# Optimization experiments

Measured on AMD Instinct MI355X. Metric: run time of the kernel, lower is better.

## Reference

```python
import jax, jax.numpy as jnp
import numpy as np

# ---- static configuration (mirrors RPN init + FPN anchor generator) ----
IMG_H = 800; IMG_W = 800
STRIDES = [4, 8, 16, 32, 64]
FEAT_SIZES = [(200, 200), (100, 100), (50, 50), (25, 25), (13, 13)]
SCALES = [32.0, 64.0, 128.0, 256.0, 512.0]
RATIOS = [0.5, 1.0, 2.0]
NUM_ANCHORS_PER_LEVEL = [len(RATIOS) * h * w for h, w in FEAT_SIZES]
A_TOTAL = sum(NUM_ANCHORS_PER_LEVEL)  # 159882
BATCH = 4
PRE_NMS_TOP_N = 1000   # _pre_nms_top_n['testing']
POST_NMS_TOP_N = 1000  # _post_nms_top_n['testing']
NMS_THRESH = 0.7
SCORE_THRESH = 0.0
MIN_SIZE = 0.001
BBOX_XFORM_CLIP = float(np.log(1000.0 / 16.0))  # torchvision BoxCoder clamp


def make_anchors():
    out = []
    for (fh, fw), stride, scale in zip(FEAT_SIZES, STRIDES, SCALES):
        base = np.array([[-scale * np.sqrt(1.0 / ar) / 2, -scale * np.sqrt(ar) / 2,
                          scale * np.sqrt(1.0 / ar) / 2, scale * np.sqrt(ar) / 2]
                         for ar in RATIOS], np.float32)  # [A,4]
        sx = (np.arange(fw, dtype=np.float32) + 0.5) * stride
        sy = (np.arange(fh, dtype=np.float32) + 0.5) * stride
        yy, xx = np.meshgrid(sy, sx, indexing='ij')
        shifts = np.stack([xx, yy, xx, yy], axis=-1).reshape(-1, 1, 4)  # [HW,1,4]
        out.append((shifts + base[None]).reshape(-1, 4))  # (H,W,A) ordering
    return np.concatenate(out, axis=0).astype(np.float32)


def setup_inputs() -> dict:
    key = jax.random.key(0)
    k1, k2 = jax.random.split(key)
    objectness = jax.random.normal(k1, (BATCH, A_TOTAL), jnp.float32)
    pred_bbox_deltas = 0.2 * jax.random.normal(k2, (BATCH, A_TOTAL, 4), jnp.float32)
    anchors = jnp.asarray(make_anchors())
    return {"objectness": objectness, "pred_bbox_deltas": pred_bbox_deltas, "anchors": anchors}


def decode_boxes(deltas, anchors):
    # BoxCoder.decode with weights (1,1,1,1)
    wa = anchors[:, 2] - anchors[:, 0]
    ha = anchors[:, 3] - anchors[:, 1]
    cxa = anchors[:, 0] + 0.5 * wa
    cya = anchors[:, 1] + 0.5 * ha
    dx, dy = deltas[..., 0], deltas[..., 1]
    dw = jnp.minimum(deltas[..., 2], BBOX_XFORM_CLIP)
    dh = jnp.minimum(deltas[..., 3], BBOX_XFORM_CLIP)
    cx = dx * wa + cxa
    cy = dy * ha + cya
    w = jnp.exp(dw) * wa
    h = jnp.exp(dh) * ha
    return jnp.stack([cx - 0.5 * w, cy - 0.5 * h, cx + 0.5 * w, cy + 0.5 * h], axis=-1)


def top_n_idx(obj):
    # _get_top_n_idx: per-level top-k with running offset
    idxs = []
    off = 0
    for n in NUM_ANCHORS_PER_LEVEL:
        k = min(PRE_NMS_TOP_N, n)
        _, ti = jax.lax.top_k(obj[:, off:off + n], k)
        idxs.append(ti + off)
        off += n
    return jnp.concatenate(idxs, axis=1)


def pairwise_iou(b):
    area = (b[:, 2] - b[:, 0]) * (b[:, 3] - b[:, 1])
    lt = jnp.maximum(b[:, None, :2], b[None, :, :2])
    rb = jnp.minimum(b[:, None, 2:], b[None, :, 2:])
    wh = jnp.clip(rb - lt, 0.0)
    inter = wh[..., 0] * wh[..., 1]
    return inter / (area[:, None] + area[None, :] - inter)


def nms_single(boxes, scores, levels):
    # clip_boxes_to_image
    x1 = jnp.clip(boxes[:, 0], 0.0, IMG_W)
    y1 = jnp.clip(boxes[:, 1], 0.0, IMG_H)
    x2 = jnp.clip(boxes[:, 2], 0.0, IMG_W)
    y2 = jnp.clip(boxes[:, 3], 0.0, IMG_H)
    boxes = jnp.stack([x1, y1, x2, y2], axis=-1)
    # remove_small_boxes + score_thresh, expressed as a static mask
    valid = (x2 - x1 >= MIN_SIZE) & (y2 - y1 >= MIN_SIZE) & (scores >= SCORE_THRESH)
    # batched_nms trick: offset boxes per level so cross-level IoU is 0
    max_coord = jnp.max(boxes)
    off = levels.astype(boxes.dtype) * (max_coord + 1.0)
    nb = boxes + off[:, None]
    s = jnp.where(valid, scores, -jnp.inf)
    order = jnp.argsort(-s)
    b = nb[order]
    K = b.shape[0]
    iou = pairwise_iou(b)  # [K,K]
    keep0 = valid[order]
    ar = jnp.arange(K)
    def body(i, keep):
        sup = (iou[i] > NMS_THRESH) & (ar > i)
        return jnp.where(keep[i], keep & ~sup, keep)
    keep = jax.lax.fori_loop(0, K, body, keep0)  # greedy NMS
    kept_scores = jnp.where(keep, s[order], -jnp.inf)
    sel = jnp.argsort(-kept_scores)[:POST_NMS_TOP_N]  # stable: preserves score order
    fvalid = jnp.take(keep, sel)
    fb = jnp.take(boxes[order], sel, axis=0)
    fs = jnp.take(scores[order], sel)
    fb = jnp.where(fvalid[:, None], fb, 0.0)  # pad slots zeroed
    fs = jnp.where(fvalid, fs, 0.0)
    return fb, fs


def reference(objectness, pred_bbox_deltas, anchors):
    proposals = decode_boxes(pred_bbox_deltas, anchors)  # [N, A, 4]
    idx = top_n_idx(objectness)  # [N, K]
    levels = jnp.concatenate([jnp.full((n,), i, jnp.int32)
                              for i, n in enumerate(NUM_ANCHORS_PER_LEVEL)])
    bi = jnp.arange(objectness.shape[0])[:, None]
    sc = jax.nn.sigmoid(objectness[bi, idx])
    lv = levels[idx]
    pr = proposals[bi, idx]
    boxes, scores = jax.vmap(nms_single)(pr, sc, lv)
    return boxes, scores  # [N, POST_NMS_TOP_N, 4], [N, POST_NMS_TOP_N]
```

## Files before the change

### kernel.cpp

```cpp
#include <hip/hip_runtime.h>
#include <math.h>

#define BATCH 4
#define A_TOTAL 159882
#define K_TOT 4507
#define N_WORDS 71
#define POST_N 1000

#define OFF_SEL      0u
#define OFF_SKEY     72192u
#define OFF_BOXES    216576u
#define OFF_SCORE    505088u
#define OFF_MAXC     577280u
#define OFF_BOXESS   577536u
#define OFF_NBS      866048u
#define OFF_SCORES   1154560u
#define OFF_SUPINIT  1226752u
#define OFF_MASK     1229056u

__device__ const int d_LVL_N[5]   = {120000, 30000, 7500, 1875, 507};
__device__ const int d_LVL_OFF[5] = {0, 120000, 150000, 157500, 159375};
__device__ const int d_LVL_K[5]   = {1000, 1000, 1000, 1000, 507};
__device__ const int d_CAT_OFF[5] = {0, 1000, 2000, 3000, 4000};

__device__ __forceinline__ float fadd_(float a, float b) { return __fadd_rn(a, b); }
__device__ __forceinline__ float fsub_(float a, float b) { return __fadd_rn(a, -b); }
__device__ __forceinline__ float fmul_(float a, float b) { return __fmul_rn(a, b); }

__device__ __forceinline__ unsigned flipf(float f) {
  unsigned u = __float_as_uint(f);
  return (u & 0x80000000u) ? ~u : (u | 0x80000000u);
}

__device__ __forceinline__ unsigned long long readlane64(unsigned long long v, int l) {
  unsigned lo = (unsigned)__builtin_amdgcn_readlane((int)(unsigned)(v & 0xffffffffull), l);
  unsigned hi = (unsigned)__builtin_amdgcn_readlane((int)(unsigned)(v >> 32), l);
  return ((unsigned long long)hi << 32) | (unsigned long long)lo;
}

__device__ __forceinline__ unsigned long long shflxor64(unsigned long long v, int msk) {
  unsigned lo = __shfl_xor((unsigned)(v & 0xffffffffull), msk, 64);
  unsigned hi = __shfl_xor((unsigned)(v >> 32), msk, 64);
  return ((unsigned long long)hi << 32) | (unsigned long long)lo;
}

__device__ void suffix_and_find(unsigned* hist, unsigned kcur,
                                unsigned* s_bucket, unsigned* s_knew, int tid) {
  for (int off = 1; off < 2048; off <<= 1) {
    unsigned v0 = hist[tid] + ((tid + off) < 2048 ? hist[tid + off] : 0u);
    unsigned v1 = hist[tid + 1024] + ((tid + 1024 + off) < 2048 ? hist[tid + 1024 + off] : 0u);
    __syncthreads();
    hist[tid] = v0; hist[tid + 1024] = v1;
    __syncthreads();
  }
  for (int q = 0; q < 2; ++q) {
    int idx = tid + q * 1024;
    unsigned s0 = hist[idx];
    unsigned s1 = (idx + 1 < 2048) ? hist[idx + 1] : 0u;
    if (s0 >= kcur && s1 < kcur) { *s_bucket = (unsigned)idx; *s_knew = kcur - s1; }
  }
  __syncthreads();
}

__global__ __launch_bounds__(1024) void topk_kernel(const float* __restrict__ obj,
                                                    int* __restrict__ selAnchor) {
  __shared__ unsigned hist[2048];
  __shared__ unsigned long long buf[2048];
  __shared__ unsigned s_bucket, s_knew, s_cnt;
  const int tid = threadIdx.x;
  const int bid = blockIdx.x;
  const int b = bid / 5, l = bid % 5;
  const int n = d_LVL_N[l];
  const int aoff = d_LVL_OFF[l];
  const unsigned kk = (unsigned)d_LVL_K[l];
  const float* src = obj + (size_t)b * A_TOTAL + aoff;

  hist[tid] = 0; hist[tid + 1024] = 0;
  __syncthreads();
  for (int i = tid; i < n; i += 1024) atomicAdd(&hist[flipf(src[i]) >> 21], 1u);
  __syncthreads();
  suffix_and_find(hist, kk, &s_bucket, &s_knew, tid);
  unsigned B1 = s_bucket, k2 = s_knew;
  __syncthreads();

  hist[tid] = 0; hist[tid + 1024] = 0;
  __syncthreads();
  for (int i = tid; i < n; i += 1024) {
    unsigned u = flipf(src[i]);
    if ((u >> 21) == B1) atomicAdd(&hist[(u >> 10) & 2047u], 1u);
  }
  __syncthreads();
  suffix_and_find(hist, k2, &s_bucket, &s_knew, tid);
  unsigned B2 = s_bucket, k3 = s_knew;
  __syncthreads();

  hist[tid] = 0; hist[tid + 1024] = 0;
  __syncthreads();
  unsigned pfx = (B1 << 11) | B2;
  for (int i = tid; i < n; i += 1024) {
    unsigned u = flipf(src[i]);
    if ((u >> 10) == pfx) atomicAdd(&hist[u & 1023u], 1u);
  }
  __syncthreads();
  suffix_and_find(hist, k3, &s_bucket, &s_knew, tid);
  unsigned T = (pfx << 10) | s_bucket;

  if (tid == 0) s_cnt = 0;
  __syncthreads();
  for (int i = tid; i < n; i += 1024) {
    unsigned u = flipf(src[i]);
    if (u >= T) {
      unsigned p = atomicAdd(&s_cnt, 1u);
      if (p < 2048u) buf[p] = ((unsigned long long)u << 32) | (unsigned long long)(~(unsigned)i);
    }
  }
  __syncthreads();
  unsigned cnt = s_cnt; if (cnt > 2048u) cnt = 2048u;
  for (int i = tid; i < 2048; i += 1024) if ((unsigned)i >= cnt) buf[i] = 0ull;
  for (unsigned kq = 2; kq <= 2048; kq <<= 1) {
    for (unsigned j = kq >> 1; j; j >>= 1) {
      __syncthreads();
      unsigned t = (unsigned)tid;
      unsigned i0 = ((t & ~(j - 1)) << 1) | (t & (j - 1));
      unsigned i1 = i0 | j;
      unsigned long long a = buf[i0], c = buf[i1];
      bool up = ((i0 & kq) == 0);
      if (up ? (a < c) : (a > c)) { buf[i0] = c; buf[i1] = a; }
    }
  }
  __syncthreads();
  if ((unsigned)tid < kk) {
    unsigned long long key = buf[tid];
    unsigned lidx = ~(unsigned)(key & 0xffffffffull);
    selAnchor[b * K_TOT + d_CAT_OFF[l] + tid] = aoff + (int)lidx;
  }
}

__global__ __launch_bounds__(512) void decode_kernel(
    const float* __restrict__ obj, const float* __restrict__ deltas,
    const float* __restrict__ anchors, const int* __restrict__ selAnchor,
    unsigned long long* __restrict__ skey, float4* __restrict__ boxes,
    float* __restrict__ score, float* __restrict__ maxc) {
  __shared__ float red[512];
  const int b = blockIdx.x;
  const int tid = threadIdx.x;
  float mymax = 0.0f;
  for (int pos = tid; pos < K_TOT; pos += 512) {
    int a = selAnchor[b * K_TOT + pos];
    float4 an = ((const float4*)anchors)[a];
    float4 dl = ((const float4*)deltas)[(size_t)b * A_TOTAL + a];
    float o = obj[(size_t)b * A_TOTAL + a];
    float wa = fsub_(an.z, an.x), ha = fsub_(an.w, an.y);
    float cxa = fadd_(an.x, fmul_(0.5f, wa));
    float cya = fadd_(an.y, fmul_(0.5f, ha));
    const float CLIP = (float)4.135166556742356;
    float dw = fminf(dl.z, CLIP), dh = fminf(dl.w, CLIP);
    float cx = fadd_(fmul_(dl.x, wa), cxa);
    float cy = fadd_(fmul_(dl.y, ha), cya);
    float w = fmul_((float)exp((double)dw), wa);
    float h = fmul_((float)exp((double)dh), ha);
    float x1 = fsub_(cx, fmul_(0.5f, w));
    float y1 = fsub_(cy, fmul_(0.5f, h));
    float x2 = fadd_(cx, fmul_(0.5f, w));
    float y2 = fadd_(cy, fmul_(0.5f, h));
    x1 = fminf(fmaxf(x1, 0.f), 800.f);
    y1 = fminf(fmaxf(y1, 0.f), 800.f);
    x2 = fminf(fmaxf(x2, 0.f), 800.f);
    y2 = fminf(fmaxf(y2, 0.f), 800.f);
    bool valid = (fsub_(x2, x1) >= 0.001f) && (fsub_(y2, y1) >= 0.001f);
    float s = (float)(1.0 / (1.0 + exp(-(double)o)));
    boxes[b * K_TOT + pos] = make_float4(x1, y1, x2, y2);
    score[b * K_TOT + pos] = s;
    float sm = valid ? s : -INFINITY;
    skey[b * K_TOT + pos] =
        ((unsigned long long)flipf(sm) << 32) | (unsigned long long)(~(unsigned)pos);
    mymax = fmaxf(mymax, fmaxf(fmaxf(x1, y1), fmaxf(x2, y2)));
  }
  red[tid] = mymax;
  __syncthreads();
  for (int s2 = 256; s2 > 0; s2 >>= 1) {
    if (tid < s2) red[tid] = fmaxf(red[tid], red[tid + s2]);
    __syncthreads();
  }
  if (tid == 0) maxc[b] = red[0];
}

__global__ __launch_bounds__(1024) void sort_kernel(
    const unsigned long long* __restrict__ skey, const float4* __restrict__ boxes,
    const float* __restrict__ score, const float* __restrict__ maxc,
    float4* __restrict__ boxesS, float4* __restrict__ nbS,
    float* __restrict__ scoreS, unsigned long long* __restrict__ supInit) {
  __shared__ unsigned long long keys[8192];
  const int b = blockIdx.x;
  const int tid = threadIdx.x;
  for (int t = tid; t < 8192; t += 1024)
    keys[t] = (t < K_TOT) ? skey[b * K_TOT + t] : 0ull;
  for (unsigned kq = 2; kq <= 8192; kq <<= 1) {
    for (unsigned j = kq >> 1; j; j >>= 1) {
      __syncthreads();
      for (unsigned t = (unsigned)tid; t < 4096; t += 1024) {
        unsigned i0 = ((t & ~(j - 1)) << 1) | (t & (j - 1));
        unsigned i1 = i0 | j;
        unsigned long long a = keys[i0], c = keys[i1];
        bool up = ((i0 & kq) == 0);
        if (up ? (a < c) : (a > c)) { keys[i0] = c; keys[i1] = a; }
      }
    }
  }
  __syncthreads();
  float mc1 = fadd_(maxc[b], 1.0f);
  for (int t = tid; t < 8192; t += 1024) {
    unsigned long long key = keys[t];
    bool inr = t < K_TOT;
    unsigned pos = ~(unsigned)(key & 0xffffffffull);
    bool valid = inr && ((unsigned)(key >> 32) != 0x007FFFFFu);
    if (inr) {
      float4 bx = boxes[b * K_TOT + pos];
      boxesS[b * K_TOT + t] = bx;
      int lvl = (int)(pos / 1000u);
      float offv = fmul_((float)lvl, mc1);
      nbS[b * K_TOT + t] = make_float4(fadd_(bx.x, offv), fadd_(bx.y, offv),
                                       fadd_(bx.z, offv), fadd_(bx.w, offv));
      scoreS[b * K_TOT + t] = score[b * K_TOT + pos];
    }
    unsigned long long bal = __ballot(valid);
    if (t < N_WORDS * 64 && (threadIdx.x & 63) == 0)
      supInit[b * N_WORDS + (t >> 6)] = ~bal;
  }
}

__global__ __launch_bounds__(64) void mask_kernel(const float4* __restrict__ nbS,
                                                  unsigned long long* __restrict__ mask) {
  const int b = blockIdx.y;
  int rem = blockIdx.x;
  int ib = 0;
  while (rem >= N_WORDS - ib) { rem -= (N_WORDS - ib); ++ib; }
  const int jb = ib + rem;
  __shared__ float4 jbox[64];
  __shared__ float jarea[64];
  const int lane = threadIdx.x;
  const int j0 = jb * 64;
  {
    int jj = j0 + lane;
    float4 bj = (jj < K_TOT) ? nbS[(size_t)b * K_TOT + jj]
                             : make_float4(-1e30f, -1e30f, -1e30f, -1e30f);
    jbox[lane] = bj;
    jarea[lane] = fmul_(fsub_(bj.z, bj.x), fsub_(bj.w, bj.y));
  }
  __syncthreads();
  const int i = ib * 64 + lane;
  if (i >= K_TOT) return;
  float4 bi = nbS[(size_t)b * K_TOT + i];
  float ai = fmul_(fsub_(bi.z, bi.x), fsub_(bi.w, bi.y));
  unsigned long long bits = 0ull;
  int jmax = K_TOT - j0; if (jmax > 64) jmax = 64;
  for (int q = 0; q < jmax; ++q) {
    int j = j0 + q;
    if (j <= i) continue;
    float4 bj = jbox[q];
    float ltx = fmaxf(bi.x, bj.x), lty = fmaxf(bi.y, bj.y);
    float rbx = fminf(bi.z, bj.z), rby = fminf(bi.w, bj.w);
    float wx = fmaxf(fsub_(rbx, ltx), 0.f), wy = fmaxf(fsub_(rby, lty), 0.f);
    float inter = fmul_(wx, wy);
    float uni = fsub_(fadd_(ai, jarea[q]), inter);
    float iou = inter / uni;
    if (iou > 0.7f) bits |= (1ull << q);
  }
  mask[((size_t)b * K_TOT + i) * N_WORDS + jb] = bits;
}

__global__ __launch_bounds__(64, 1) void scan_kernel(
    const unsigned long long* __restrict__ mask,
    const unsigned long long* __restrict__ supInit,
    const float4* __restrict__ boxesS, const float* __restrict__ scoreS,
    float* __restrict__ out) {
  __shared__ unsigned short keptIdx[POST_N];
  const int b = blockIdx.x;
  const int lane = threadIdx.x;
  const unsigned long long* m = mask + (size_t)b * K_TOT * N_WORDS;
  unsigned long long supA = supInit[b * N_WORDS + lane];
  unsigned long long supB = (lane < N_WORDS - 64) ? supInit[b * N_WORDS + 64 + lane] : ~0ull;
  float4* ob = (float4*)(out + (size_t)b * POST_N * 4);
  float* os = out + 4 * POST_N * 4 + (size_t)b * POST_N;
  const int lane2 = (lane + 64 < N_WORDS) ? (lane + 64) : lane;
  int c = 0;
  unsigned long long rw_cur = (lane < K_TOT) ? m[(size_t)lane * N_WORDS] : 0ull;
  for (int w = 0; w < N_WORDS; ++w) {
    unsigned long long rw_next = 0ull;
    if (w + 1 < N_WORDS) {
      int i1 = (w + 1) * 64 + lane;
      if (i1 < K_TOT) rw_next = m[(size_t)i1 * N_WORDS + (w + 1)];
    }
    if (w == 64) {
      for (int j = 0; j < N_WORDS - 64; ++j) {
        unsigned long long acc = 0ull;
        for (int base = 0; base < c; base += 64) {
          int k2 = base + lane;
          unsigned long long v2 = 0ull;
          if (k2 < c) v2 = m[(size_t)keptIdx[k2] * N_WORDS + 64 + j];
          acc |= v2;
        }
        for (int msk = 32; msk > 0; msk >>= 1) acc |= shflxor64(acc, msk);
        if (lane == j) supB |= acc;
      }
    }
    unsigned long long v = (w < 64) ? supA : supB;
    int srcl = (w < 64) ? w : (w - 64);
    unsigned long long scur = readlane64(v, srcl);
    unsigned long long avail0 = ~scur;
    unsigned long long keptm = 0ull;

    if (w < 64) {
      int tq[64];
      unsigned long long dA[64];
      unsigned long long av = avail0;
      if (avail0) {
#pragma unroll
        for (int q = 0; q < 64; ++q) {
          unsigned long long avq = av ? av : 1ull;
          tq[q] = __builtin_ctzll(avq);
          av &= av - 1ull;
          const unsigned long long* rp = m + (size_t)(w * 64 + tq[q]) * N_WORDS;
          asm volatile("global_load_dwordx2 %0, %1, off" : "=&v"(dA[q]) : "v"(rp + lane));
        }
      }
      __builtin_amdgcn_sched_barrier(0);
      unsigned long long avail = avail0;
      while (avail) {
        int t = __builtin_ctzll(avail);
        keptm |= (1ull << t);
        unsigned long long rw = readlane64(rw_cur, t);
        avail &= ~(rw | (1ull << t));
      }
      int nk = __popcll(keptm);
      if (keptm) {
        int pos = c + (int)__popcll(keptm & ((1ull << lane) - 1ull));
        if (((keptm >> lane) & 1ull) && pos < POST_N)
          keptIdx[pos] = (unsigned short)(w * 64 + lane);
      }
      c += nk;
      if (c >= POST_N) break;
      if (avail0) {
        asm volatile("s_waitcnt vmcnt(0)" ::: "memory");
        __builtin_amdgcn_sched_barrier(0);
        unsigned long long acc0 = 0ull;
#pragma unroll
        for (int q = 0; q < 64; ++q) {
          unsigned long long sel = ((keptm >> tq[q]) & 1ull) ? ~0ull : 0ull;
          acc0 |= dA[q] & sel;
        }
        supA |= acc0;
      }
    } else {
      unsigned long long avail = avail0;
      while (avail) {
        int t = __builtin_ctzll(avail);
        keptm |= (1ull << t);
        unsigned long long rw = readlane64(rw_cur, t);
        avail &= ~(rw | (1ull << t));
      }
      int nk = __popcll(keptm);
      if (keptm) {
        int pos = c + (int)__popcll(keptm & ((1ull << lane) - 1ull));
        if (((keptm >> lane) & 1ull) && pos < POST_N)
          keptIdx[pos] = (unsigned short)(w * 64 + lane);
      }
      c += nk;
      if (c >= POST_N) break;
      if (w + 1 >= N_WORDS) break;
      unsigned long long km = keptm;
      while (km != 0ull) {
        int ts[16];
        unsigned long long vm[16];
#pragma unroll
        for (int q = 0; q < 16; ++q) {
          unsigned long long kms = km ? km : 1ull;
          ts[q] = __builtin_ctzll(kms);
          vm[q] = km ? ~0ull : 0ull;
          km &= km - 1ull;
        }
        unsigned long long dA2[16], dB2[16];
#pragma unroll
        for (int q = 0; q < 16; ++q) {
          const unsigned long long* row = m + (size_t)(w * 64 + ts[q]) * N_WORDS;
          dA2[q] = row[lane];
          dB2[q] = row[lane2];
        }
        __builtin_amdgcn_sched_barrier(0);
        unsigned long long acc0 = 0ull, acc1 = 0ull;
#pragma unroll
        for (int q = 0; q < 16; ++q) {
          acc0 |= dA2[q] & vm[q];
          acc1 |= dB2[q] & vm[q];
        }
        supA |= acc0; supB |= acc1;
      }
    }
    rw_cur = rw_next;
  }
  __syncthreads();
  for (int t2 = lane; t2 < c && t2 < POST_N; t2 += 64) {
    int i = keptIdx[t2];
    ob[t2] = boxesS[(size_t)b * K_TOT + i];
    os[t2] = scoreS[(size_t)b * K_TOT + i];
  }
  for (int t2 = (c < POST_N ? c : POST_N) + lane; t2 < POST_N; t2 += 64) {
    ob[t2] = make_float4(0.f, 0.f, 0.f, 0.f);
    os[t2] = 0.f;
  }
}

extern "C" void kernel_launch(void* const* d_in, const int* in_sizes, int n_in,
                              void* d_out, int out_size, void* d_ws, size_t ws_size,
                              hipStream_t stream) {
  const float* obj = (const float*)d_in[0];
  const float* deltas = (const float*)d_in[1];
  const float* anchors = (const float*)d_in[2];
  float* out = (float*)d_out;
  char* ws = (char*)d_ws;

  int* selAnchor = (int*)(ws + OFF_SEL);
  unsigned long long* skey = (unsigned long long*)(ws + OFF_SKEY);
  float4* boxes = (float4*)(ws + OFF_BOXES);
  float* score = (float*)(ws + OFF_SCORE);
  float* maxc = (float*)(ws + OFF_MAXC);
  float4* boxesS = (float4*)(ws + OFF_BOXESS);
  float4* nbS = (float4*)(ws + OFF_NBS);
  float* scoreS = (float*)(ws + OFF_SCORES);
  unsigned long long* supInit = (unsigned long long*)(ws + OFF_SUPINIT);
  unsigned long long* mask = (unsigned long long*)(ws + OFF_MASK);

  hipLaunchKernelGGL(topk_kernel, dim3(BATCH * 5), dim3(1024), 0, stream, obj, selAnchor);
  hipLaunchKernelGGL(decode_kernel, dim3(BATCH), dim3(512), 0, stream,
                     obj, deltas, anchors, selAnchor, skey, boxes, score, maxc);
  hipLaunchKernelGGL(sort_kernel, dim3(BATCH), dim3(1024), 0, stream,
                     skey, boxes, score, maxc, boxesS, nbS, scoreS, supInit);
  hipLaunchKernelGGL(mask_kernel, dim3(N_WORDS * (N_WORDS + 1) / 2, BATCH), dim3(64), 0, stream,
                     nbS, mask);
  hipLaunchKernelGGL(scan_kernel, dim3(BATCH), dim3(64), 0, stream,
                     mask, supInit, boxesS, scoreS, out);
}
```

Baseline: 423.8 us.

## Rework top-k selection: replicated histograms, wave scan, rank-sort instead of bitonic

The per-level top-k kernel now spreads the first histogram pass over four padded copies to cut atomic contention. The block-wide suffix scan is replaced by a single-wave scan with shuffles. Candidates are split into strict-greater and tie sets, ties resolved by index with a wave min-reduction. The final order comes from an O(k^2) rank count instead of a 2048-element bitonic sort. This removes many block barriers but adds quadratic shared reads per thread and a serial tie-resolution loop when ties occur.

```diff
diff --git a/kernel.cpp b/kernel.cpp
--- a/kernel.cpp
+++ b/kernel.cpp
@@ -44,29 +44,44 @@
   return ((unsigned long long)hi << 32) | (unsigned long long)lo;
 }
 
-__device__ void suffix_and_find(unsigned* hist, unsigned kcur,
-                                unsigned* s_bucket, unsigned* s_knew, int tid) {
-  for (int off = 1; off < 2048; off <<= 1) {
-    unsigned v0 = hist[tid] + ((tid + off) < 2048 ? hist[tid + off] : 0u);
-    unsigned v1 = hist[tid + 1024] + ((tid + 1024 + off) < 2048 ? hist[tid + 1024 + off] : 0u);
-    __syncthreads();
-    hist[tid] = v0; hist[tid + 1024] = v1;
-    __syncthreads();
-  }
-  for (int q = 0; q < 2; ++q) {
-    int idx = tid + q * 1024;
-    unsigned s0 = hist[idx];
-    unsigned s1 = (idx + 1 < 2048) ? hist[idx + 1] : 0u;
-    if (s0 >= kcur && s1 < kcur) { *s_bucket = (unsigned)idx; *s_knew = kcur - s1; }
+#define HCOPIES 4
+#define HSTRIDE 2049
+#define TIE_CAP 2048
+
+__device__ __forceinline__ void suffix_find_wave(const unsigned* hist, unsigned kcur,
+                                                 unsigned* s_bucket, unsigned* s_knew,
+                                                 int tid) {
+  if (tid < 64) {
+    const int lane = tid;
+    unsigned ch[32];
+    unsigned csum = 0;
+#pragma unroll
+    for (int j = 0; j < 32; ++j) { ch[j] = hist[lane * 32 + j]; csum += ch[j]; }
+    unsigned cs = csum;
+    for (int off = 1; off < 64; off <<= 1) {
+      unsigned nb = __shfl_down(cs, off, 64);
+      cs += (lane + off < 64) ? nb : 0u;
+    }
+    unsigned running = cs - csum;
+#pragma unroll
+    for (int j = 31; j >= 0; --j) {
+      unsigned newrun = running + ch[j];
+      if (newrun >= kcur && running < kcur) {
+        *s_bucket = (unsigned)(lane * 32 + j);
+        *s_knew = kcur - running;
+      }
+      running = newrun;
+    }
   }
   __syncthreads();
 }
 
 __global__ __launch_bounds__(1024) void topk_kernel(const float* __restrict__ obj,
                                                     int* __restrict__ selAnchor) {
-  __shared__ unsigned hist[2048];
-  __shared__ unsigned long long buf[2048];
-  __shared__ unsigned s_bucket, s_knew, s_cnt;
+  __shared__ unsigned hist[HCOPIES * HSTRIDE];
+  __shared__ unsigned tieA[TIE_CAP];
+  __shared__ unsigned long long selK[1024];
+  __shared__ unsigned s_bucket, s_knew, s_ngt, s_ntie;
   const int tid = threadIdx.x;
   const int bid = blockIdx.x;
   const int b = bid / 5, l = bid % 5;
@@ -74,27 +89,33 @@
   const int aoff = d_LVL_OFF[l];
   const unsigned kk = (unsigned)d_LVL_K[l];
   const float* src = obj + (size_t)b * A_TOTAL + aoff;
-
-  hist[tid] = 0; hist[tid + 1024] = 0;
-  __syncthreads();
-  for (int i = tid; i < n; i += 1024) atomicAdd(&hist[flipf(src[i]) >> 21], 1u);
-  __syncthreads();
-  suffix_and_find(hist, kk, &s_bucket, &s_knew, tid);
+  int* outp = selAnchor + b * K_TOT + d_CAT_OFF[l];
+  const int wcopy = (tid >> 6) & (HCOPIES - 1);
+
+  for (int i = tid; i < HCOPIES * HSTRIDE; i += 1024) hist[i] = 0;
+  __syncthreads();
+  for (int i = tid; i < n; i += 1024)
+    atomicAdd(&hist[wcopy * HSTRIDE + (flipf(src[i]) >> 21)], 1u);
+  __syncthreads();
+  for (int i = tid; i < 2048; i += 1024)
+    hist[i] = hist[i] + hist[HSTRIDE + i] + hist[2 * HSTRIDE + i] + hist[3 * HSTRIDE + i];
+  __syncthreads();
+  suffix_find_wave(hist, kk, &s_bucket, &s_knew, tid);
   unsigned B1 = s_bucket, k2 = s_knew;
   __syncthreads();
 
-  hist[tid] = 0; hist[tid + 1024] = 0;
+  for (int i = tid; i < 2048; i += 1024) hist[i] = 0;
   __syncthreads();
   for (int i = tid; i < n; i += 1024) {
     unsigned u = flipf(src[i]);
     if ((u >> 21) == B1) atomicAdd(&hist[(u >> 10) & 2047u], 1u);
   }
   __syncthreads();
-  suffix_and_find(hist, k2, &s_bucket, &s_knew, tid);
+  suffix_find_wave(hist, k2, &s_bucket, &s_knew, tid);
   unsigned B2 = s_bucket, k3 = s_knew;
   __syncthreads();
 
-  hist[tid] = 0; hist[tid + 1024] = 0;
+  for (int i = tid; i < 2048; i += 1024) hist[i] = 0;
   __syncthreads();
   unsigned pfx = (B1 << 11) | B2;
   for (int i = tid; i < n; i += 1024) {
@@ -102,37 +123,57 @@
     if ((u >> 10) == pfx) atomicAdd(&hist[u & 1023u], 1u);
   }
   __syncthreads();
-  suffix_and_find(hist, k3, &s_bucket, &s_knew, tid);
+  suffix_find_wave(hist, k3, &s_bucket, &s_knew, tid);
   unsigned T = (pfx << 10) | s_bucket;
 
-  if (tid == 0) s_cnt = 0;
+  if (tid == 0) { s_ngt = 0; s_ntie = 0; }
   __syncthreads();
   for (int i = tid; i < n; i += 1024) {
     unsigned u = flipf(src[i]);
-    if (u >= T) {
-      unsigned p = atomicAdd(&s_cnt, 1u);
-      if (p < 2048u) buf[p] = ((unsigned long long)u << 32) | (unsigned long long)(~(unsigned)i);
-    }
-  }
-  __syncthreads();
-  unsigned cnt = s_cnt; if (cnt > 2048u) cnt = 2048u;
-  for (int i = tid; i < 2048; i += 1024) if ((unsigned)i >= cnt) buf[i] = 0ull;
-  for (unsigned kq = 2; kq <= 2048; kq <<= 1) {
-    for (unsigned j = kq >> 1; j; j >>= 1) {
-      __syncthreads();
-      unsigned t = (unsigned)tid;
-      unsigned i0 = ((t & ~(j - 1)) << 1) | (t & (j - 1));
-      unsigned i1 = i0 | j;
-      unsigned long long a = buf[i0], c = buf[i1];
-      bool up = ((i0 & kq) == 0);
-      if (up ? (a < c) : (a > c)) { buf[i0] = c; buf[i1] = a; }
-    }
-  }
-  __syncthreads();
-  if ((unsigned)tid < kk) {
-    unsigned long long key = buf[tid];
-    unsigned lidx = ~(unsigned)(key & 0xffffffffull);
-    selAnchor[b * K_TOT + d_CAT_OFF[l] + tid] = aoff + (int)lidx;
+    if (u > T) {
+      unsigned p = atomicAdd(&s_ngt, 1u);
+      selK[p] = ((unsigned long long)u << 32) | (unsigned)(~(unsigned)i);
+    } else if (u == T) {
+      unsigned q = atomicAdd(&s_ntie, 1u);
+      if (q < TIE_CAP) tieA[q] = (unsigned)i;
+    }
+  }
+  __syncthreads();
+  const unsigned ngt = s_ngt, ntie = s_ntie;
+  const unsigned need = kk - ngt;
+  if (ntie == need) {
+    for (unsigned q = tid; q < ntie; q += 1024)
+      selK[ngt + q] = ((unsigned long long)T << 32) | (unsigned)(~tieA[q]);
+  } else if (tid < 64) {
+    const int lane = tid;
+    int prev = -1;
+    for (unsigned r = 0; r < need; ++r) {
+      unsigned best = 0xFFFFFFFFu;
+      if (ntie <= TIE_CAP) {
+        for (unsigned j = lane; j < ntie; j += 64) {
+          unsigned cand = tieA[j];
+          if ((int)cand > prev && cand < best) best = cand;
+        }
+      } else {
+        for (int j = lane; j < n; j += 64)
+          if (flipf(src[j]) == T && j > prev && (unsigned)j < best) best = (unsigned)j;
+      }
+      for (int off = 32; off; off >>= 1) {
+        unsigned o = __shfl_xor(best, off, 64);
+        best = best < o ? best : o;
+      }
+      if (lane == 0) selK[ngt + r] = ((unsigned long long)T << 32) | (unsigned)(~best);
+      prev = (int)best;
+    }
+  }
+  __syncthreads();
+
+  if (tid < (int)kk) {
+    const unsigned long long mykey = selK[tid];
+    unsigned r = 0;
+    for (unsigned j = 0; j < kk; ++j) r += (selK[j] > mykey) ? 1u : 0u;
+    unsigned myIdx = ~(unsigned)(mykey & 0xffffffffull);
+    outp[r] = aoff + (int)myIdx;
   }
 }
 
```

Result: no change. 428.9 us (+1.2%).
